# Kernel optimization log

Measured on AMD Instinct MI355X. Metric: run time of the kernel, lower is better.

Reference implementation:

```python
import jax, jax.numpy as jnp
import numpy as np

N_NODES, HIDDEN, LATENT, T_STEPS, BATCH, N_HEADS, N_LAYERS = 512, 64, 256, 10, 64, 4, 2
LN_EPS = 1e-5


def _layer_norm(x, g, b):
    mu = x.mean(-1, keepdims=True)
    var = ((x - mu) ** 2).mean(-1, keepdims=True)
    return (x - mu) * jax.lax.rsqrt(var + LN_EPS) * g + b


def _encoder_layer(x, in_w, in_b, out_w, out_b, l1_w, l1_b, l2_w, l2_b, g1, b1, g2, b2):
    # x: [S, B, D]; post-LN torch TransformerEncoderLayer, relu, no dropout (eval)
    S, B, D = x.shape
    hd = D // N_HEADS
    qkv = x @ in_w + in_b
    q, k, v = jnp.split(qkv, 3, axis=-1)
    q = q.reshape(S, B, N_HEADS, hd)
    k = k.reshape(S, B, N_HEADS, hd)
    v = v.reshape(S, B, N_HEADS, hd)
    att = jax.nn.softmax(jnp.einsum('sbhd,tbhd->bhst', q, k) / jnp.sqrt(jnp.float32(hd)), axis=-1)
    o = jnp.einsum('bhst,tbhd->sbhd', att, v).reshape(S, B, D) @ out_w + out_b
    x = _layer_norm(x + o, g1, b1)
    ff = jax.nn.relu(x @ l1_w + l1_b) @ l2_w + l2_b
    return _layer_norm(x + ff, g2, b2)


def _gru(x, w_ih, w_hh, b_ih, b_hh):
    # x: [B, T, I]; torch GRU gate order (r, z, n); returns all hidden states [B, T, H]
    Hh = w_hh.shape[0]
    gi = x @ w_ih + b_ih  # [B, T, 3H]

    def step(h, gi_t):
        gh = h @ w_hh + b_hh
        ir, iz, inn = jnp.split(gi_t, 3, -1)
        hr, hz, hn = jnp.split(gh, 3, -1)
        r = jax.nn.sigmoid(ir + hr)
        z = jax.nn.sigmoid(iz + hz)
        n = jnp.tanh(inn + r * hn)
        h_new = (1.0 - z) * n + z * h
        return h_new, h_new

    h0 = jnp.zeros((x.shape[0], Hh), x.dtype)
    _, out = jax.lax.scan(step, h0, jnp.swapaxes(gi, 0, 1))
    return jnp.swapaxes(out, 0, 1)


def _replace_zero(t):
    return jnp.where(t == 0.0, jnp.asarray(1e-8, t.dtype), t)


def _forward(X, Z, edge_score_now, edge_score_lag, prior_adj, wp1, bp1, enc_in_w, enc_in_b, enc_out_w, enc_out_b, enc_l1_w, enc_l1_b, enc_l2_w, enc_l2_b, enc_g1, enc_b1, enc_g2, enc_b2, wp2, bp2, fs_w, fs_b, ft_w, ft_b, gru_w_ih, gru_w_hh, gru_b_ih, gru_b_hh, tp_w, tp_b, ltn_w, ltn_b, gat_wl, gat_bl, gat_wr, gat_br, gat_att, gat_bias, gl_w, gl_b, time_context):
    # --- transformer encoder over time ---
    x = X @ wp1 + bp1                       # [B, T, H]
    x = jnp.transpose(x, (1, 0, 2))          # [T, B, H] (seq-first)
    for l in range(N_LAYERS):
        x = _encoder_layer(x, enc_in_w[l], enc_in_b[l], enc_out_w[l], enc_out_b[l], enc_l1_w[l], enc_l1_b[l], enc_l2_w[l], enc_l2_b[l], enc_g1[l], enc_b1[l], enc_g2[l], enc_b2[l])
    x = x @ wp2 + bp2                        # [T, B, N]
    x_inst = x[0]
    x_lag = x[1:].mean(0)
    # --- gumbel-softmax adjacency (tau=1, hard=False); fixed gumbel noise key ---
    k1, k2 = jax.random.split(jax.random.key(42))
    log_now = jnp.einsum('bk,bj->kj', x_inst, x_inst)
    log_lag = jax.nn.sigmoid(jnp.einsum('bk,bj->kj', x_lag, x_lag))
    a_now = jax.nn.softmax(log_now + jax.random.gumbel(k1, log_now.shape, log_now.dtype), -1)
    a_lag = jax.nn.softmax(log_lag + jax.random.gumbel(k2, log_lag.shape, log_lag.dtype), -1)
    adj_now = jnp.clip(jax.nn.sigmoid(edge_score_now + prior_adj + a_now), 0.0, 1.0)
    adj_lag = jnp.clip(jax.nn.sigmoid(edge_score_lag + prior_adj + a_lag), 0.0, 1.0)
    eye = jnp.eye(adj_now.shape[0], dtype=bool)
    adj_now = _replace_zero(jnp.where(eye, 0.0, adj_now))
    adj_lag = _replace_zero(jnp.where(eye, 0.0, adj_lag))
    # --- temporal RealNVP flow ---
    z1, z2 = jnp.split(Z, 2, axis=1)
    s = jax.nn.sigmoid(z1 @ fs_w + fs_b)
    z2 = s * z2 + (z1 @ ft_w + ft_b)
    freqs = jnp.exp(jnp.linspace(0.0, float(T_STEPS), LATENT // 2)).astype(Z.dtype)
    sin_in = time_context.astype(Z.dtype)[..., None] * freqs      # [N, T, L/2]
    temb = jnp.concatenate([jnp.sin(sin_in), jnp.cos(sin_in)], -1)  # [N, T, L]
    tout = _gru(temb, gru_w_ih, gru_w_hh, gru_b_ih, gru_b_hh)      # [N, T, L/2]
    z2 = z2 + jnp.einsum('btc,t->bc', tout, tp_w) + tp_b
    Zn = jnp.concatenate([z1, z2], 1) @ ltn_w + ltn_b              # [N, num_nodes]
    # --- GATv2 message passing; adj_now+adj_lag has no exact zeros (replace_zero),
    # so dense_to_sparse yields the fully connected edge set incl. self-loops ---
    Hh, C = gat_att.shape
    Nn = Zn.shape[0]
    xl = (Zn @ gat_wl + gat_bl).reshape(Nn, Hh, C)  # source features
    xr = (Zn @ gat_wr + gat_br).reshape(Nn, Hh, C)  # target features
    e = jnp.einsum('ijhc,hc->ijh', jax.nn.leaky_relu(xr[:, None] + xl[None, :], 0.2), gat_att)
    alpha = jax.nn.softmax(e, axis=1)                # softmax over source nodes j
    x_emb = jnp.einsum('ijh,jhc->ihc', alpha, xl).reshape(Nn, Hh * C) + gat_bias
    ml = x_emb @ gl_w + gl_b
    mean, log_var = jnp.split(ml, 2, -1)
    scale = jnp.exp(0.5 * jnp.clip(log_var, -5.0, 2.0))  # Laplace(mean, scale) params
    return adj_now, adj_lag, mean, scale


def setup_inputs() -> dict:
    key = jax.random.key(0)
    ks = iter(jax.random.split(key, 64))

    def rn(shape, scale=1.0):
        return jax.random.normal(next(ks), shape, jnp.float32) * scale

    N, Hd, L, T, B, nL = N_NODES, HIDDEN, LATENT, T_STEPS, BATCH, N_LAYERS
    d3 = 3 * Hd
    inp = dict(
        X=rn((B, T, N)),
        Z=rn((N, L)),
        edge_score_now=rn((N, N)),
        edge_score_lag=rn((N, N)),
        prior_adj=jnp.zeros((N, N), jnp.float32),
        wp1=rn((N, Hd), N ** -0.5), bp1=jnp.zeros((Hd,), jnp.float32),
        enc_in_w=rn((nL, Hd, d3), Hd ** -0.5), enc_in_b=jnp.zeros((nL, d3), jnp.float32),
        enc_out_w=rn((nL, Hd, Hd), Hd ** -0.5), enc_out_b=jnp.zeros((nL, Hd), jnp.float32),
        enc_l1_w=rn((nL, Hd, Hd), Hd ** -0.5), enc_l1_b=jnp.zeros((nL, Hd), jnp.float32),
        enc_l2_w=rn((nL, Hd, Hd), Hd ** -0.5), enc_l2_b=jnp.zeros((nL, Hd), jnp.float32),
        enc_g1=jnp.ones((nL, Hd), jnp.float32), enc_b1=jnp.zeros((nL, Hd), jnp.float32),
        enc_g2=jnp.ones((nL, Hd), jnp.float32), enc_b2=jnp.zeros((nL, Hd), jnp.float32),
        wp2=rn((Hd, N), Hd ** -0.5), bp2=jnp.zeros((N,), jnp.float32),
        fs_w=rn((L // 2, L // 2), (L // 2) ** -0.5), fs_b=jnp.zeros((L // 2,), jnp.float32),
        ft_w=rn((L // 2, L // 2), (L // 2) ** -0.5), ft_b=jnp.zeros((L // 2,), jnp.float32),
        gru_w_ih=rn((L, 3 * (L // 2)), L ** -0.5),
        gru_w_hh=rn((L // 2, 3 * (L // 2)), (L // 2) ** -0.5),
        gru_b_ih=jnp.zeros((3 * (L // 2),), jnp.float32),
        gru_b_hh=jnp.zeros((3 * (L // 2),), jnp.float32),
        tp_w=rn((T,), T ** -0.5), tp_b=jnp.zeros((1,), jnp.float32),
        ltn_w=rn((L, N), L ** -0.5), ltn_b=jnp.zeros((N,), jnp.float32),
        gat_wl=rn((N, 4 * Hd), N ** -0.5), gat_bl=jnp.zeros((4 * Hd,), jnp.float32),
        gat_wr=rn((N, 4 * Hd), N ** -0.5), gat_br=jnp.zeros((4 * Hd,), jnp.float32),
        gat_att=rn((4, Hd), Hd ** -0.5), gat_bias=jnp.zeros((4 * Hd,), jnp.float32),
        gl_w=rn((4 * Hd, 2 * N), (4 * Hd) ** -0.5), gl_b=jnp.zeros((2 * N,), jnp.float32),
        time_context=jax.random.randint(next(ks), (N, T), 0, 100, jnp.int32),
    )
    return inp


def reference(X, Z, edge_score_now, edge_score_lag, prior_adj, wp1, bp1, enc_in_w, enc_in_b, enc_out_w, enc_out_b, enc_l1_w, enc_l1_b, enc_l2_w, enc_l2_b, enc_g1, enc_b1, enc_g2, enc_b2, wp2, bp2, fs_w, fs_b, ft_w, ft_b, gru_w_ih, gru_w_hh, gru_b_ih, gru_b_hh, tp_w, tp_b, ltn_w, ltn_b, gat_wl, gat_bl, gat_wr, gat_br, gat_att, gat_bias, gl_w, gl_b, time_context):
    return _forward(X, Z, edge_score_now, edge_score_lag, prior_adj, wp1, bp1, enc_in_w, enc_in_b, enc_out_w, enc_out_b, enc_l1_w, enc_l1_b, enc_l2_w, enc_l2_b, enc_g1, enc_b1, enc_g2, enc_b2, wp2, bp2, fs_w, fs_b, ft_w, ft_b, gru_w_ih, gru_w_hh, gru_b_ih, gru_b_hh, tp_w, tp_b, ltn_w, ltn_b, gat_wl, gat_bl, gat_wr, gat_br, gat_att, gat_bias, gl_w, gl_b, time_context)
```

## Files before the change

### kernel.cpp

```cpp
#include <hip/hip_runtime.h>
#include <stdint.h>
#include <math.h>

#define NN 512
#define HID 64
#define LAT 256
#define TS 10
#define BAT 64

#define DEVFN static __device__ __forceinline__

DEVFN uint32_t rotl32(uint32_t v, int d) { return (v << d) | (v >> (32 - d)); }

DEVFN void threefry2x32(uint32_t k0, uint32_t k1, uint32_t x0, uint32_t x1,
                        uint32_t& o0, uint32_t& o1) {
  uint32_t ks0 = k0, ks1 = k1, ks2 = k0 ^ k1 ^ 0x1BD11BDAu;
  x0 += ks0; x1 += ks1;
  x0 += x1; x1 = rotl32(x1, 13); x1 ^= x0;
  x0 += x1; x1 = rotl32(x1, 15); x1 ^= x0;
  x0 += x1; x1 = rotl32(x1, 26); x1 ^= x0;
  x0 += x1; x1 = rotl32(x1, 6);  x1 ^= x0;
  x0 += ks1; x1 += ks2 + 1u;
  x0 += x1; x1 = rotl32(x1, 17); x1 ^= x0;
  x0 += x1; x1 = rotl32(x1, 29); x1 ^= x0;
  x0 += x1; x1 = rotl32(x1, 16); x1 ^= x0;
  x0 += x1; x1 = rotl32(x1, 24); x1 ^= x0;
  x0 += ks2; x1 += ks0 + 2u;
  x0 += x1; x1 = rotl32(x1, 13); x1 ^= x0;
  x0 += x1; x1 = rotl32(x1, 15); x1 ^= x0;
  x0 += x1; x1 = rotl32(x1, 26); x1 ^= x0;
  x0 += x1; x1 = rotl32(x1, 6);  x1 ^= x0;
  x0 += ks0; x1 += ks1 + 3u;
  x0 += x1; x1 = rotl32(x1, 17); x1 ^= x0;
  x0 += x1; x1 = rotl32(x1, 29); x1 ^= x0;
  x0 += x1; x1 = rotl32(x1, 16); x1 ^= x0;
  x0 += x1; x1 = rotl32(x1, 24); x1 ^= x0;
  x0 += ks1; x1 += ks2 + 4u;
  x0 += x1; x1 = rotl32(x1, 13); x1 ^= x0;
  x0 += x1; x1 = rotl32(x1, 15); x1 ^= x0;
  x0 += x1; x1 = rotl32(x1, 26); x1 ^= x0;
  x0 += x1; x1 = rotl32(x1, 6);  x1 ^= x0;
  x0 += ks2; x1 += ks0 + 5u;
  o0 = x0; o1 = x1;
}

DEVFN float sigmoidf_(float x) { return 1.0f / (1.0f + expf(-x)); }

DEVFN float gumbel_bits(uint32_t bits) {
  const float tiny = 1.17549435e-38f;
  float f = __uint_as_float((bits >> 9) | 0x3F800000u) - 1.0f;
  float u = f * (1.0f - tiny) + tiny;
  u = fmaxf(tiny, u);
  return -logf(-logf(u));
}

DEVFN float block_red256(float v, float* red, bool ismax) {
  #pragma unroll
  for (int o = 32; o > 0; o >>= 1) {
    float w = __shfl_down(v, o, 64);
    v = ismax ? fmaxf(v, w) : v + w;
  }
  if ((threadIdx.x & 63) == 0) red[threadIdx.x >> 6] = v;
  __syncthreads();
  float r = ismax ? fmaxf(fmaxf(red[0], red[1]), fmaxf(red[2], red[3]))
                  : ((red[0] + red[1]) + (red[2] + red[3]));
  __syncthreads();
  return r;
}

DEVFN float wave_red_sum64(float v) {
  #pragma unroll
  for (int o = 32; o > 0; o >>= 1) v += __shfl_xor(v, o, 64);
  return v;
}

#define ACC4(acc, x4, w4) { acc += (x4).x * (w4).x; acc += (x4).y * (w4).y; \
                            acc += (x4).z * (w4).z; acc += (x4).w * (w4).w; }

__global__ __launch_bounds__(384) void prep_kernel(
    const float* __restrict__ w_hh, float* __restrict__ w_hhT,
    const float* __restrict__ X, const float* __restrict__ wp1,
    const float* __restrict__ bp1, float* __restrict__ x0,
    const float* __restrict__ w_ih, const float* __restrict__ b_ih,
    float* __restrict__ gi_table,
    const float* __restrict__ Z, const float* __restrict__ fs_w,
    const float* __restrict__ fs_b, const float* __restrict__ ft_w,
    const float* __restrict__ ft_b, float* __restrict__ z2p) {
  const int tid = threadIdx.x;
  if (blockIdx.x < 128) {
    const int idx = blockIdx.x * 384 + tid;
    const int k4 = idx / 1536, rem = idx % 1536;
    const int t = rem >> 2, kl = rem & 3;
    w_hhT[idx] = w_hh[(k4 * 4 + kl) * 384 + t];
  } else if (blockIdx.x < 288) {
    const int r0 = (blockIdx.x - 128) * 4;
    const int g = tid >> 6, c = tid & 63;
    __shared__ float Xb[4][NN];
    __shared__ float Wb[128 * 64];
    for (int i = tid; i < 4 * NN; i += 384)
      Xb[i >> 9][i & 511] = X[r0 * NN + i];
    float acc = (tid < 256) ? bp1[c] : 0.0f;
    for (int ch = 0; ch < 4; ch++) {
      const int n0 = ch * 128;
      __syncthreads();
      for (int i = tid; i < 128 * 64; i += 384) {
        int k = i >> 6, cc = i & 63;
        Wb[((k >> 2) * 64 + cc) * 4 + (k & 3)] = wp1[(n0 + k) * 64 + cc];
      }
      __syncthreads();
      if (tid < 256) {
        #pragma unroll 8
        for (int n4 = 0; n4 < 32; n4++) {
          float4 w4 = *(const float4*)&Wb[(n4 * 64 + c) * 4];
          float4 x4 = *(const float4*)&Xb[g][n0 + n4 * 4];
          ACC4(acc, x4, w4);
        }
      }
    }
    if (tid < 256) x0[(r0 + g) * HID + c] = acc;
  } else if (blockIdx.x < 388) {
    const int v = blockIdx.x - 288;
    const int t = tid;
    __shared__ float temb[256];
    if (t < 256) {
      float fr = (float)exp((double)(t & 127) * (10.0 / 127.0));
      float arg = (float)v * fr;
      temb[t] = (t < 128) ? sinf(arg) : cosf(arg);
    }
    __syncthreads();
    float acc = b_ih[t];
    for (int k = 0; k < 256; k++) acc += temb[k] * w_ih[k * 384 + t];
    gi_table[v * 384 + t] = acc;
  } else {
    const int n = (blockIdx.x - 388) * 3 + (tid >> 7);
    const int c = tid & 127;
    __shared__ float z1s[3][128];
    if (n < NN) z1s[tid >> 7][c] = Z[n * LAT + c];
    __syncthreads();
    if (n < NN) {
      const float* z1 = z1s[tid >> 7];
      float a = fs_b[c], t = ft_b[c];
      for (int k = 0; k < 128; k++) {
        float zz = z1[k];
        a += zz * fs_w[k * 128 + c];
        t += zz * ft_w[k * 128 + c];
      }
      z2p[n * 128 + c] = sigmoidf_(a) * Z[n * LAT + 128 + c] + t;
    }
  }
}

__global__ __launch_bounds__(768) void encgru_kernel(
    const float* __restrict__ x0,
    const float* __restrict__ in_w, const float* __restrict__ in_b,
    const float* __restrict__ out_w, const float* __restrict__ out_b,
    const float* __restrict__ l1_w, const float* __restrict__ l1_b,
    const float* __restrict__ l2_w, const float* __restrict__ l2_b,
    const float* __restrict__ g1, const float* __restrict__ b1,
    const float* __restrict__ g2, const float* __restrict__ b2,
    float* __restrict__ x_enc,
    const int* __restrict__ tctx, const float* __restrict__ w_hhT4,
    const float* __restrict__ b_hh, const float* __restrict__ gi_table,
    const float* __restrict__ tp_w, const float* __restrict__ tp_b,
    const float* __restrict__ z2p, float* __restrict__ z2f) {
  __shared__ float smem[28176];
  const int tid = threadIdx.x;

  if (blockIdx.x < 64) {
    const int b = blockIdx.x;
    const int s = tid >> 6, c = tid & 63;
    float* WbA  = smem;
    float* WbB  = smem + 12288;
    float* xx   = smem + 24576;
    float* qkv  = smem + 25216;
    float* scb  = smem + 27136;
    float* tmpv = smem + 27536;

    if (tid < 640) xx[s * 64 + c] = x0[b * 640 + tid];

    for (int l = 0; l < 2; l++) {
      const float* inw = in_w + l * HID * 192; const float* inb = in_b + l * 192;
      const float* ow  = out_w + l * HID * HID; const float* ob = out_b + l * HID;
      const float* w1  = l1_w + l * HID * HID; const float* bb1 = l1_b + l * HID;
      const float* w2  = l2_w + l * HID * HID; const float* bb2 = l2_b + l * HID;
      const float* gg1 = g1 + l * HID; const float* be1 = b1 + l * HID;
      const float* gg2 = g2 + l * HID; const float* be2 = b2 + l * HID;

      __syncthreads();
      for (int i = tid; i < 12288; i += 768) {
        int k = i / 192, cc = i % 192;
        WbA[((k >> 2) * 192 + cc) * 4 + (k & 3)] = inw[i];
      }
      for (int i = tid; i < 12288; i += 768) {
        int m = i >> 12, rem = i & 4095, k = rem >> 6, cc = rem & 63;
        float v = (m == 0) ? ow[rem] : (m == 1) ? w1[rem] : w2[rem];
        WbB[m * 4096 + ((k >> 2) * 64 + cc) * 4 + (k & 3)] = v;
      }
      __syncthreads();

      if (tid < 640) {
        #pragma unroll
        for (int part = 0; part < 3; part++) {
          const int cc = part * 64 + c;
          float acc = inb[cc];
          #pragma unroll
          for (int k4 = 0; k4 < 16; k4++) {
            float4 w4 = *(const float4*)&WbA[(k4 * 192 + cc) * 4];
            float4 x4 = *(const float4*)&xx[s * 64 + k4 * 4];
            ACC4(acc, x4, w4);
          }
          qkv[s * 192 + cc] = acc;
        }
      }
      __syncthreads();

      if (tid < 40) {
        const int h = tid / 10, r = tid % 10;
        float e[10];
        for (int t = 0; t < 10; t++) {
          float acc = 0.0f;
          for (int d = 0; d < 16; d++)
            acc += qkv[r * 192 + h * 16 + d] * qkv[t * 192 + 64 + h * 16 + d];
          e[t] = acc * 0.25f;
        }
        float m = -1e30f;
        for (int t = 0; t < 10; t++) m = fmaxf(m, e[t]);
        float sum = 0.0f;
        for (int t = 0; t < 10; t++) { e[t] = expf(e[t] - m); sum += e[t]; }
        float inv = 1.0f / sum;
        for (int t = 0; t < 10; t++) scb[h * 100 + r * 10 + t] = e[t] * inv;
      }
      __syncthreads();

      float v1 = 0.0f;
      if (tid < 640) {
        const int h = c >> 4;
        float acc = 0.0f;
        for (int t = 0; t < 10; t++)
          acc += scb[h * 100 + s * 10 + t] * qkv[t * 192 + 128 + c];
        tmpv[s * 64 + c] = acc;
      }
      __threadfence_block();
      if (tid < 640) {
        float acc = ob[c] + xx[s * 64 + c];
        #pragma unroll
        for (int k4 = 0; k4 < 16; k4++) {
          float4 w4 = *(const float4*)&WbB[(k4 * 64 + c) * 4];
          float4 x4 = *(const float4*)&tmpv[s * 64 + k4 * 4];
          ACC4(acc, x4, w4);
        }
        float mu = wave_red_sum64(acc) * (1.0f / 64.0f);
        float d = acc - mu;
        float var = wave_red_sum64(d * d) * (1.0f / 64.0f);
        float rs = rsqrtf(var + 1e-5f);
        v1 = d * rs * gg1[c] + be1[c];
        xx[s * 64 + c] = v1;
      }
      __threadfence_block();
      if (tid < 640) {
        float acc = bb1[c];
        #pragma unroll
        for (int k4 = 0; k4 < 16; k4++) {
          float4 w4 = *(const float4*)&WbB[4096 + (k4 * 64 + c) * 4];
          float4 x4 = *(const float4*)&xx[s * 64 + k4 * 4];
          ACC4(acc, x4, w4);
        }
        tmpv[s * 64 + c] = fmaxf(acc, 0.0f);
      }
      __threadfence_block();
      if (tid < 640) {
        float acc = bb2[c] + v1;
        #pragma unroll
        for (int k4 = 0; k4 < 16; k4++) {
          float4 w4 = *(const float4*)&WbB[8192 + (k4 * 64 + c) * 4];
          float4 x4 = *(const float4*)&tmpv[s * 64 + k4 * 4];
          ACC4(acc, x4, w4);
        }
        float mu = wave_red_sum64(acc) * (1.0f / 64.0f);
        float d = acc - mu;
        float var = wave_red_sum64(d * d) * (1.0f / 64.0f);
        float rs = rsqrtf(var + 1e-5f);
        xx[s * 64 + c] = d * rs * gg2[c] + be2[c];
      }
      __threadfence_block();
    }
    if (tid < 640) x_enc[b * 640 + tid] = xx[s * 64 + c];
  } else {
    const int n0 = (blockIdx.x - 64) * 4;
    const int half = tid >= 384 ? 1 : 0;
    const int c = tid - half * 384;
    float* h      = smem;
    float* part   = smem + 512;
    float* gi_lds = smem + 3584;
    float* tpw    = smem + 18944;
    for (int i = tid; i < 4 * TS * 384; i += 768) {
      int g = i / 3840, rem = i % 3840, s = rem / 384, col = rem % 384;
      gi_lds[(g * TS + s) * 384 + col] = gi_table[tctx[(n0 + g) * 10 + s] * 384 + col];
    }
    if (tid < TS) tpw[tid] = tp_w[tid];
    const float4* wbase = (const float4*)w_hhT4 + (half * 16) * 384 + c;
    const float bhh = (half == 0) ? b_hh[c] : 0.0f;
    float acc_tp = 0.0f;
    if (tid < 512) h[tid] = 0.0f;
    __syncthreads();
    #pragma unroll
    for (int s = 0; s < 10; s++) {
      float accs[4];
      #pragma unroll
      for (int g = 0; g < 4; g++) accs[g] = bhh;
      #pragma unroll
      for (int k4 = 0; k4 < 16; k4++) {
        float4 w4 = wbase[k4 * 384];
        #pragma unroll
        for (int g = 0; g < 4; g++) {
          float4 hv = *(const float4*)&h[g * 128 + (half * 16 + k4) * 4];
          ACC4(accs[g], hv, w4);
        }
      }
      #pragma unroll
      for (int g = 0; g < 4; g++) part[(half * 4 + g) * 384 + c] = accs[g];
      __syncthreads();
      if (tid < 512) {
        const int g = tid >> 7, cc = tid & 127;
        const float* gi = gi_lds + (g * TS + s) * 384;
        float gh_r = part[g * 384 + cc]           + part[(4 + g) * 384 + cc];
        float gh_z = part[g * 384 + 128 + cc]     + part[(4 + g) * 384 + 128 + cc];
        float gh_n = part[g * 384 + 256 + cc]     + part[(4 + g) * 384 + 256 + cc];
        float r = sigmoidf_(gi[cc] + gh_r);
        float z = sigmoidf_(gi[128 + cc] + gh_z);
        float nn2 = tanhf(gi[256 + cc] + r * gh_n);
        float hn = (1.0f - z) * nn2 + z * h[g * 128 + cc];
        h[g * 128 + cc] = hn;
        acc_tp += hn * tpw[s];
      }
      __syncthreads();
    }
    if (tid < 512) {
      const int g = tid >> 7, cc = tid & 127;
      z2f[(n0 + g) * 128 + cc] = z2p[(n0 + g) * 128 + cc] + acc_tp + tp_b[0];
    }
  }
}

__global__ __launch_bounds__(256) void wp2zna_kernel(
    const float* __restrict__ x_enc, const float* __restrict__ wp2,
    const float* __restrict__ bp2,
    float* __restrict__ x_inst, float* __restrict__ x_lag,
    const float* __restrict__ Z, const float* __restrict__ z2f,
    const float* __restrict__ ltn_w, const float* __restrict__ ltn_b,
    float* __restrict__ zn_ws) {
  const int tid = threadIdx.x;
  if (blockIdx.x < 128) {
    const int b = blockIdx.x >> 1, half = blockIdx.x & 1;
    const int n = half * 256 + tid;
    __shared__ float xxl[640];
    __shared__ float Wb[32 * 256];
    for (int i = tid; i < 640; i += 256) xxl[i] = x_enc[b * 640 + i];
    float accs[10];
    #pragma unroll
    for (int si = 0; si < 10; si++) accs[si] = 0.0f;
    for (int ch = 0; ch < 2; ch++) {
      __syncthreads();
      for (int i = tid; i < 32 * 256; i += 256)
        Wb[i] = wp2[(ch * 32 + (i >> 8)) * NN + half * 256 + (i & 255)];
      __syncthreads();
      for (int k = 0; k < 32; k++) {
        float w = Wb[k * 256 + tid];
        #pragma unroll
        for (int si = 0; si < 10; si++) accs[si] += xxl[si * 64 + ch * 32 + k] * w;
      }
    }
    float bias = bp2[n];
    x_inst[b * NN + n] = accs[0] + bias;
    float lag = 0.0f;
    for (int si = 1; si < 10; si++) lag += accs[si];
    x_lag[b * NN + n] = lag * (1.0f / 9.0f) + bias;
  } else {
    const int bid = blockIdx.x - 128;
    const int nt = bid >> 2, cg = bid & 3;
    const int oo = tid & 127, gsel = tid >> 7;
    const int o = cg * 128 + oo;
    const int n0 = nt * 4;
    __shared__ float zcat[4][LAT];
    for (int i = tid; i < 4 * LAT; i += 256) {
      int g = i >> 8, k = i & 255;
      zcat[g][k] = (k < 128) ? Z[(n0 + g) * LAT + k] : z2f[(n0 + g) * 128 + (k - 128)];
    }
    __syncthreads();
    const float bias = ltn_b[o];
    float accA = bias, accB = bias;
    const int g0 = gsel, g1 = gsel + 2;
    for (int k = 0; k < LAT; k++) {
      float w = ltn_w[k * NN + o];
      accA += zcat[g0][k] * w;
      accB += zcat[g1][k] * w;
    }
    zn_ws[(n0 + g0) * NN + o] = accA;
    zn_ws[(n0 + g1) * NN + o] = accB;
  }
}

__global__ __launch_bounds__(256) void adjznb_kernel(
    const float* __restrict__ x_inst, const float* __restrict__ x_lag,
    const float* __restrict__ es_now, const float* __restrict__ es_lag,
    const float* __restrict__ prior, float* __restrict__ out,
    const float* __restrict__ zn_ws,
    const float* __restrict__ wl, const float* __restrict__ bl,
    const float* __restrict__ wr, const float* __restrict__ br,
    float* __restrict__ xl, float* __restrict__ xr) {
  const int tid = threadIdx.x;
  if (blockIdx.x < 1024) {
    const int k = blockIdx.x & 511;
    const int v = blockIdx.x >> 9;
    const float* xs = v ? x_lag : x_inst;
    const float* es = v ? es_lag : es_now;
    __shared__ float ck[BAT];
    __shared__ float red[4];
    if (tid < BAT) ck[tid] = xs[tid * NN + k];
    __syncthreads();
    uint32_t ka, kb, t0, t1;
    threefry2x32(0u, 42u, 0u, (uint32_t)v, ka, kb);
    float vals[2];
    #pragma unroll
    for (int jj = 0; jj < 2; jj++) {
      int j = tid + jj * 256;
      float acc = 0.0f;
      for (int bb = 0; bb < BAT; bb++) acc += ck[bb] * xs[bb * NN + j];
      if (v) acc = sigmoidf_(acc);
      threefry2x32(ka, kb, 0u, (uint32_t)(k * NN + j), t0, t1);
      vals[jj] = acc + gumbel_bits(t0 ^ t1);
    }
    float m = block_red256(fmaxf(vals[0], vals[1]), red, true);
    float e0 = expf(vals[0] - m), e1 = expf(vals[1] - m);
    float s = block_red256(e0 + e1, red, false);
    float inv = 1.0f / s;
    #pragma unroll
    for (int jj = 0; jj < 2; jj++) {
      int j = tid + jj * 256;
      float a = (jj ? e1 : e0) * inv;
      float t = es[k * NN + j] + prior[k * NN + j] + a;
      float sg = sigmoidf_(t);
      sg = fminf(fmaxf(sg, 0.0f), 1.0f);
      if (j == k) sg = 0.0f;
      if (sg == 0.0f) sg = 1e-8f;
      out[v * NN * NN + k * NN + j] = sg;
    }
  } else {
    const int bid = blockIdx.x - 1024;
    const int nt = bid >> 2, cg = bid & 3;
    const int o = cg * 64 + (tid & 63), g = tid >> 6;
    const int n = nt * 4 + g;
    __shared__ float znr[4][NN];
    for (int i = tid; i < 4 * NN; i += 256)
      znr[i >> 9][i & 511] = zn_ws[(nt * 4 + (i >> 9)) * NN + (i & 511)];
    __syncthreads();
    float accL = bl[o], accR = br[o];
    for (int k = 0; k < NN; k++) {
      float z = znr[g][k];
      accL += z * wl[k * 256 + o];
      accR += z * wr[k * 256 + o];
    }
    xl[n * 256 + o] = accL;
    xr[n * 256 + o] = accR;
  }
}

__global__ __launch_bounds__(256) void gatE4_kernel(
    const float* __restrict__ xl, const float* __restrict__ xr,
    const float* __restrict__ attw, float* __restrict__ e_ws) {
  const int b = blockIdx.x;
  const int jt = b & 7, h = (b >> 3) & 3, it = b >> 5;
  const int tid = threadIdx.x;
  const int i_l = tid >> 4, jq = tid & 15;
  __shared__ float xlt[64][68];
  __shared__ float xrt[16][68];
  __shared__ float awl[64];
  for (int idx = tid; idx < 1024; idx += 256) {
    int j = idx >> 4, c4 = idx & 15;
    float4 v = *(const float4*)&xl[(jt * 64 + j) * 256 + h * 64 + c4 * 4];
    xlt[c4 * 4 + 0][j] = v.x;
    xlt[c4 * 4 + 1][j] = v.y;
    xlt[c4 * 4 + 2][j] = v.z;
    xlt[c4 * 4 + 3][j] = v.w;
  }
  for (int idx = tid; idx < 1024; idx += 256) {
    int i = idx >> 6, cc = idx & 63;
    xrt[i][cc] = xr[(it * 16 + i) * 256 + h * 64 + cc];
  }
  if (tid < 64) awl[tid] = attw[h * 64 + tid];
  __syncthreads();
  float acc0 = 0.0f, acc1 = 0.0f, acc2 = 0.0f, acc3 = 0.0f;
  #pragma unroll
  for (int c4 = 0; c4 < 16; c4++) {
    float4 aw4 = *(const float4*)&awl[c4 * 4];
    float4 xr4 = *(const float4*)&xrt[i_l][c4 * 4];
    float4 xl0 = *(const float4*)&xlt[c4 * 4 + 0][jq * 4];
    float4 xl1 = *(const float4*)&xlt[c4 * 4 + 1][jq * 4];
    float4 xl2 = *(const float4*)&xlt[c4 * 4 + 2][jq * 4];
    float4 xl3 = *(const float4*)&xlt[c4 * 4 + 3][jq * 4];
    {
      float v0 = xr4.x + xl0.x; v0 = (v0 >= 0.0f) ? v0 : 0.2f * v0;
      float v1 = xr4.x + xl0.y; v1 = (v1 >= 0.0f) ? v1 : 0.2f * v1;
      float v2 = xr4.x + xl0.z; v2 = (v2 >= 0.0f) ? v2 : 0.2f * v2;
      float v3 = xr4.x + xl0.w; v3 = (v3 >= 0.0f) ? v3 : 0.2f * v3;
      acc0 += v0 * aw4.x; acc1 += v1 * aw4.x; acc2 += v2 * aw4.x; acc3 += v3 * aw4.x;
    }
    {
      float v0 = xr4.y + xl1.x; v0 = (v0 >= 0.0f) ? v0 : 0.2f * v0;
      float v1 = xr4.y + xl1.y; v1 = (v1 >= 0.0f) ? v1 : 0.2f * v1;
      float v2 = xr4.y + xl1.z; v2 = (v2 >= 0.0f) ? v2 : 0.2f * v2;
      float v3 = xr4.y + xl1.w; v3 = (v3 >= 0.0f) ? v3 : 0.2f * v3;
      acc0 += v0 * aw4.y; acc1 += v1 * aw4.y; acc2 += v2 * aw4.y; acc3 += v3 * aw4.y;
    }
    {
      float v0 = xr4.z + xl2.x; v0 = (v0 >= 0.0f) ? v0 : 0.2f * v0;
      float v1 = xr4.z + xl2.y; v1 = (v1 >= 0.0f) ? v1 : 0.2f * v1;
      float v2 = xr4.z + xl2.z; v2 = (v2 >= 0.0f) ? v2 : 0.2f * v2;
      float v3 = xr4.z + xl2.w; v3 = (v3 >= 0.0f) ? v3 : 0.2f * v3;
      acc0 += v0 * aw4.z; acc1 += v1 * aw4.z; acc2 += v2 * aw4.z; acc3 += v3 * aw4.z;
    }
    {
      float v0 = xr4.w + xl3.x; v0 = (v0 >= 0.0f) ? v0 : 0.2f * v0;
      float v1 = xr4.w + xl3.y; v1 = (v1 >= 0.0f) ? v1 : 0.2f * v1;
      float v2 = xr4.w + xl3.z; v2 = (v2 >= 0.0f) ? v2 : 0.2f * v2;
      float v3 = xr4.w + xl3.w; v3 = (v3 >= 0.0f) ? v3 : 0.2f * v3;
      acc0 += v0 * aw4.w; acc1 += v1 * aw4.w; acc2 += v2 * aw4.w; acc3 += v3 * aw4.w;
    }
  }
  const int i = it * 16 + i_l;
  float* dst = e_ws + i * 2048 + h * 512 + jt * 64 + jq * 4;
  dst[0] = acc0; dst[1] = acc1; dst[2] = acc2; dst[3] = acc3;
}

__global__ __launch_bounds__(256) void gatSX_kernel(
    const float* __restrict__ e_ws, const float* __restrict__ xl,
    const float* __restrict__ gbias, float* __restrict__ xemb) {
  const int it = blockIdx.x >> 2, h = blockIdx.x & 3;
  const int tid = threadIdx.x;
  const int cq = tid & 15, jp = (tid >> 4) & 3, ip = tid >> 6;
  __shared__ float al[4][512];
  __shared__ float red[4];
  for (int i = tid; i < 4 * 512; i += 256)
    al[i >> 9][i & 511] = e_ws[(it * 4 + (i >> 9)) * 2048 + h * 512 + (i & 511)];
  __syncthreads();
  #pragma unroll
  for (int ii = 0; ii < 4; ii++) {
    float v0 = al[ii][tid], v1 = al[ii][256 + tid];
    float m = block_red256(fmaxf(v0, v1), red, true);
    float e0 = expf(v0 - m), e1 = expf(v1 - m);
    float ssum = block_red256(e0 + e1, red, false);
    float inv = 1.0f / ssum;
    al[ii][tid] = e0 * inv;
    al[ii][256 + tid] = e1 * inv;
  }
  __syncthreads();
  float acc0 = 0.0f, acc1 = 0.0f, acc2 = 0.0f, acc3 = 0.0f;
  #pragma unroll 4
  for (int js = 0; js < 128; js++) {
    const int j = js * 4 + jp;
    float4 x4 = *(const float4*)&xl[j * 256 + h * 64 + cq * 4];
    float a = al[ip][j];
    acc0 += a * x4.x; acc1 += a * x4.y; acc2 += a * x4.z; acc3 += a * x4.w;
  }
  acc0 += __shfl_xor(acc0, 16, 64); acc0 += __shfl_xor(acc0, 32, 64);
  acc1 += __shfl_xor(acc1, 16, 64); acc1 += __shfl_xor(acc1, 32, 64);
  acc2 += __shfl_xor(acc2, 16, 64); acc2 += __shfl_xor(acc2, 32, 64);
  acc3 += __shfl_xor(acc3, 16, 64); acc3 += __shfl_xor(acc3, 32, 64);
  if (jp == 0) {
    const int i = it * 4 + ip;
    const int o = h * 64 + cq * 4;
    float4 v = make_float4(acc0 + gbias[o],     acc1 + gbias[o + 1],
                           acc2 + gbias[o + 2], acc3 + gbias[o + 3]);
    *(float4*)&xemb[i * 256 + o] = v;
  }
}

__global__ __launch_bounds__(256) void gat_fused_kernel(
    const float* __restrict__ xl, const float* __restrict__ xr,
    const float* __restrict__ attw, const float* __restrict__ gbias,
    float* __restrict__ xemb) {
  const int i0 = blockIdx.x * 2, tid = threadIdx.x;
  __shared__ float xri[2][256];
  __shared__ float aw[256];
  __shared__ float e[2][4][NN];
  __shared__ float part[4][2][256];
  __shared__ float red[4];
  xri[0][tid] = xr[i0 * 256 + tid];
  xri[1][tid] = xr[(i0 + 1) * 256 + tid];
  aw[tid] = attw[tid];
  __syncthreads();
  #pragma unroll
  for (int jj = 0; jj < 2; jj++) {
    const int j = tid + jj * 256;
    const float4* xl4 = (const float4*)(xl + j * 256);
    #pragma unroll
    for (int hh = 0; hh < 4; hh++) {
      float accA = 0.0f, accB = 0.0f;
      #pragma unroll 4
      for (int c4 = 0; c4 < 16; c4++) {
        float4 v = xl4[hh * 16 + c4];
        const int cb = hh * 64 + c4 * 4;
        float w0 = aw[cb + 0], w1 = aw[cb + 1], w2 = aw[cb + 2], w3 = aw[cb + 3];
        float a0 = xri[0][cb + 0] + v.x; a0 = (a0 >= 0.0f) ? a0 : 0.2f * a0;
        float a1 = xri[0][cb + 1] + v.y; a1 = (a1 >= 0.0f) ? a1 : 0.2f * a1;
        float a2 = xri[0][cb + 2] + v.z; a2 = (a2 >= 0.0f) ? a2 : 0.2f * a2;
        float a3 = xri[0][cb + 3] + v.w; a3 = (a3 >= 0.0f) ? a3 : 0.2f * a3;
        accA += a0 * w0; accA += a1 * w1; accA += a2 * w2; accA += a3 * w3;
        float b0 = xri[1][cb + 0] + v.x; b0 = (b0 >= 0.0f) ? b0 : 0.2f * b0;
        float b1 = xri[1][cb + 1] + v.y; b1 = (b1 >= 0.0f) ? b1 : 0.2f * b1;
        float b2 = xri[1][cb + 2] + v.z; b2 = (b2 >= 0.0f) ? b2 : 0.2f * b2;
        float b3 = xri[1][cb + 3] + v.w; b3 = (b3 >= 0.0f) ? b3 : 0.2f * b3;
        accB += b0 * w0; accB += b1 * w1; accB += b2 * w2; accB += b3 * w3;
      }
      e[0][hh][j] = accA;
      e[1][hh][j] = accB;
    }
  }
  __syncthreads();
  for (int ii = 0; ii < 2; ii++) {
    for (int hh = 0; hh < 4; hh++) {
      float v0 = e[ii][hh][tid], v1 = e[ii][hh][tid + 256];
      float m = block_red256(fmaxf(v0, v1), red, true);
      float e0 = expf(v0 - m), e1 = expf(v1 - m);
      float ssum = block_red256(e0 + e1, red, false);
      float inv = 1.0f / ssum;
      e[ii][hh][tid] = e0 * inv;
      e[ii][hh][tid + 256] = e1 * inv;
    }
  }
  __syncthreads();
  {
    const int w = tid >> 6, lane = tid & 63;
    float a0 = 0.0f, a1 = 0.0f, a2 = 0.0f, a3 = 0.0f;
    float b0 = 0.0f, b1 = 0.0f, b2 = 0.0f, b3 = 0.0f;
    const int j0 = w * 128;
    for (int j = j0; j < j0 + 128; j++) {
      const float* xlr = xl + j * 256 + lane;
      float x0 = xlr[0], x1 = xlr[64], x2 = xlr[128], x3 = xlr[192];
      a0 += e[0][0][j] * x0; a1 += e[0][1][j] * x1;
      a2 += e[0][2][j] * x2; a3 += e[0][3][j] * x3;
      b0 += e[1][0][j] * x0; b1 += e[1][1][j] * x1;
      b2 += e[1][2][j] * x2; b3 += e[1][3][j] * x3;
    }
    part[w][0][lane]       = a0;
    part[w][0][64 + lane]  = a1;
    part[w][0][128 + lane] = a2;
    part[w][0][192 + lane] = a3;
    part[w][1][lane]       = b0;
    part[w][1][64 + lane]  = b1;
    part[w][1][128 + lane] = b2;
    part[w][1][192 + lane] = b3;
  }
  __syncthreads();
  {
    float accA = ((part[0][0][tid] + part[1][0][tid]) + part[2][0][tid]) + part[3][0][tid];
    float accB = ((part[0][1][tid] + part[1][1][tid]) + part[2][1][tid]) + part[3][1][tid];
    float gb = gbias[tid];
    xemb[i0 * 256 + tid] = accA + gb;
    xemb[(i0 + 1) * 256 + tid] = accB + gb;
  }
}

__global__ __launch_bounds__(256) void glgemm_kernel(
    const float* __restrict__ xemb, const float* __restrict__ gl_w,
    const float* __restrict__ gl_b, float* __restrict__ out_mean,
    float* __restrict__ out_scale) {
  const int ct = blockIdx.x & 15, it = blockIdx.x >> 4;
  const int tid = threadIdx.x;
  const int i0 = it * 16, col = ct * 64 + (tid & 63), ti = tid >> 6;
  __shared__ float xe[16][LAT];
  for (int o = tid; o < 16 * LAT; o += 256) {
    xe[o >> 8][o & 255] = xemb[(i0 + (o >> 8)) * LAT + (o & 255)];
  }
  __syncthreads();
  const float bias = gl_b[col];
  float acc0 = bias, acc1 = bias, acc2 = bias, acc3 = bias;
  const int r0 = ti * 4;
  #pragma unroll 4
  for (int k = 0; k < LAT; k++) {
    float w = gl_w[k * 1024 + col];
    acc0 += xe[r0 + 0][k] * w;
    acc1 += xe[r0 + 1][k] * w;
    acc2 += xe[r0 + 2][k] * w;
    acc3 += xe[r0 + 3][k] * w;
  }
  float accs[4] = {acc0, acc1, acc2, acc3};
  if (col < 512) {
    #pragma unroll
    for (int q = 0; q < 4; q++) out_mean[(i0 + r0 + q) * NN + col] = accs[q];
  } else {
    #pragma unroll
    for (int q = 0; q < 4; q++) {
      float lv = fminf(fmaxf(accs[q], -5.0f), 2.0f);
      out_scale[(i0 + r0 + q) * NN + (col - 512)] = expf(0.5f * lv);
    }
  }
}

extern "C" void kernel_launch(void* const* d_in, const int* in_sizes, int n_in,
                              void* d_out, int out_size, void* d_ws, size_t ws_size,
                              hipStream_t stream) {
  (void)in_sizes; (void)n_in; (void)out_size;
  const float* X        = (const float*)d_in[0];
  const float* Z        = (const float*)d_in[1];
  const float* es_now   = (const float*)d_in[2];
  const float* es_lag   = (const float*)d_in[3];
  const float* prior    = (const float*)d_in[4];
  const float* wp1      = (const float*)d_in[5];
  const float* bp1      = (const float*)d_in[6];
  const float* enc_in_w = (const float*)d_in[7];
  const float* enc_in_b = (const float*)d_in[8];
  const float* enc_out_w= (const float*)d_in[9];
  const float* enc_out_b= (const float*)d_in[10];
  const float* enc_l1_w = (const float*)d_in[11];
  const float* enc_l1_b = (const float*)d_in[12];
  const float* enc_l2_w = (const float*)d_in[13];
  const float* enc_l2_b = (const float*)d_in[14];
  const float* enc_g1   = (const float*)d_in[15];
  const float* enc_b1   = (const float*)d_in[16];
  const float* enc_g2   = (const float*)d_in[17];
  const float* enc_b2   = (const float*)d_in[18];
  const float* wp2      = (const float*)d_in[19];
  const float* bp2      = (const float*)d_in[20];
  const float* fs_w     = (const float*)d_in[21];
  const float* fs_b     = (const float*)d_in[22];
  const float* ft_w     = (const float*)d_in[23];
  const float* ft_b     = (const float*)d_in[24];
  const float* gru_w_ih = (const float*)d_in[25];
  const float* gru_w_hh = (const float*)d_in[26];
  const float* gru_b_ih = (const float*)d_in[27];
  const float* gru_b_hh = (const float*)d_in[28];
  const float* tp_w     = (const float*)d_in[29];
  const float* tp_b     = (const float*)d_in[30];
  const float* ltn_w    = (const float*)d_in[31];
  const float* ltn_b    = (const float*)d_in[32];
  const float* gat_wl   = (const float*)d_in[33];
  const float* gat_bl   = (const float*)d_in[34];
  const float* gat_wr   = (const float*)d_in[35];
  const float* gat_br   = (const float*)d_in[36];
  const float* gat_att  = (const float*)d_in[37];
  const float* gat_bias = (const float*)d_in[38];
  const float* gl_w     = (const float*)d_in[39];
  const float* gl_b     = (const float*)d_in[40];
  const int*   tctx     = (const int*)d_in[41];

  float* out = (float*)d_out;
  float* ws  = (float*)d_ws;
  float* x_inst   = ws;
  float* x_lag    = ws + 32768;
  float* z2p      = ws + 65536;
  float* z2f      = ws + 131072;
  float* xl       = ws + 196608;
  float* xr       = ws + 327680;
  float* gi_table = ws + 458752;
  float* xemb     = ws + 497152;
  float* x0       = ws + 628224;
  float* x_enc    = ws + 669184;
  float* zn_ws    = ws + 710144;
  float* e_ws     = ws + 972288;
  float* w_hhT4   = zn_ws;

  const bool big_ws = ws_size >= (size_t)(972288 + 512 * 2048) * 4;

  prep_kernel<<<dim3(559), dim3(384), 0, stream>>>(
      gru_w_hh, w_hhT4, X, wp1, bp1, x0,
      gru_w_ih, gru_b_ih, gi_table,
      Z, fs_w, fs_b, ft_w, ft_b, z2p);
  encgru_kernel<<<dim3(192), dim3(768), 0, stream>>>(
      x0, enc_in_w, enc_in_b, enc_out_w, enc_out_b,
      enc_l1_w, enc_l1_b, enc_l2_w, enc_l2_b,
      enc_g1, enc_b1, enc_g2, enc_b2, x_enc,
      tctx, w_hhT4, gru_b_hh, gi_table, tp_w, tp_b, z2p, z2f);
  wp2zna_kernel<<<dim3(640), dim3(256), 0, stream>>>(
      x_enc, wp2, bp2, x_inst, x_lag, Z, z2f, ltn_w, ltn_b, zn_ws);
  adjznb_kernel<<<dim3(1536), dim3(256), 0, stream>>>(
      x_inst, x_lag, es_now, es_lag, prior, out,
      zn_ws, gat_wl, gat_bl, gat_wr, gat_br, xl, xr);
  if (big_ws) {
    gatE4_kernel<<<dim3(1024), dim3(256), 0, stream>>>(xl, xr, gat_att, e_ws);
    gatSX_kernel<<<dim3(512), dim3(256), 0, stream>>>(e_ws, xl, gat_bias, xemb);
  } else {
    gat_fused_kernel<<<dim3(NN / 2), dim3(256), 0, stream>>>(
        xl, xr, gat_att, gat_bias, xemb);
  }
  glgemm_kernel<<<dim3(512), dim3(256), 0, stream>>>(
      xemb, gl_w, gl_b, out + 2 * NN * NN, out + 3 * NN * NN);
}
```

Measured before the change: 165.7 us.

## Fuse GAT attention scores, softmax, aggregation and output GEMM into one kernel

Replaces the separate GAT score, softmax/aggregate and output-linear kernels with a single kernel. Each block owns four target nodes, tiles xl through shared memory to compute edge scores, applies the softmax, aggregates, and then runs the gl_w GEMM directly from shared memory. This removes two kernel launches and the global round trips for the score matrix and xemb. The cost is only 128 blocks for the whole GAT stage, a large shared-memory footprint (about 106 KB), and every block re-reading all of xl and gl_w, which may leave the GPU under-occupied.

Measured after the change: 252.7 us. 52.5% more time.

```diff
diff --git a/kernel.cpp b/kernel.cpp
--- a/kernel.cpp
+++ b/kernel.cpp
@@ -465,234 +465,102 @@
   }
 }
 
-__global__ __launch_bounds__(256) void gatE4_kernel(
-    const float* __restrict__ xl, const float* __restrict__ xr,
-    const float* __restrict__ attw, float* __restrict__ e_ws) {
-  const int b = blockIdx.x;
-  const int jt = b & 7, h = (b >> 3) & 3, it = b >> 5;
-  const int tid = threadIdx.x;
-  const int i_l = tid >> 4, jq = tid & 15;
-  __shared__ float xlt[64][68];
-  __shared__ float xrt[16][68];
-  __shared__ float awl[64];
-  for (int idx = tid; idx < 1024; idx += 256) {
-    int j = idx >> 4, c4 = idx & 15;
-    float4 v = *(const float4*)&xl[(jt * 64 + j) * 256 + h * 64 + c4 * 4];
-    xlt[c4 * 4 + 0][j] = v.x;
-    xlt[c4 * 4 + 1][j] = v.y;
-    xlt[c4 * 4 + 2][j] = v.z;
-    xlt[c4 * 4 + 3][j] = v.w;
-  }
-  for (int idx = tid; idx < 1024; idx += 256) {
-    int i = idx >> 6, cc = idx & 63;
-    xrt[i][cc] = xr[(it * 16 + i) * 256 + h * 64 + cc];
-  }
-  if (tid < 64) awl[tid] = attw[h * 64 + tid];
-  __syncthreads();
-  float acc0 = 0.0f, acc1 = 0.0f, acc2 = 0.0f, acc3 = 0.0f;
-  #pragma unroll
-  for (int c4 = 0; c4 < 16; c4++) {
-    float4 aw4 = *(const float4*)&awl[c4 * 4];
-    float4 xr4 = *(const float4*)&xrt[i_l][c4 * 4];
-    float4 xl0 = *(const float4*)&xlt[c4 * 4 + 0][jq * 4];
-    float4 xl1 = *(const float4*)&xlt[c4 * 4 + 1][jq * 4];
-    float4 xl2 = *(const float4*)&xlt[c4 * 4 + 2][jq * 4];
-    float4 xl3 = *(const float4*)&xlt[c4 * 4 + 3][jq * 4];
-    {
-      float v0 = xr4.x + xl0.x; v0 = (v0 >= 0.0f) ? v0 : 0.2f * v0;
-      float v1 = xr4.x + xl0.y; v1 = (v1 >= 0.0f) ? v1 : 0.2f * v1;
-      float v2 = xr4.x + xl0.z; v2 = (v2 >= 0.0f) ? v2 : 0.2f * v2;
-      float v3 = xr4.x + xl0.w; v3 = (v3 >= 0.0f) ? v3 : 0.2f * v3;
-      acc0 += v0 * aw4.x; acc1 += v1 * aw4.x; acc2 += v2 * aw4.x; acc3 += v3 * aw4.x;
-    }
-    {
-      float v0 = xr4.y + xl1.x; v0 = (v0 >= 0.0f) ? v0 : 0.2f * v0;
-      float v1 = xr4.y + xl1.y; v1 = (v1 >= 0.0f) ? v1 : 0.2f * v1;
-      float v2 = xr4.y + xl1.z; v2 = (v2 >= 0.0f) ? v2 : 0.2f * v2;
-      float v3 = xr4.y + xl1.w; v3 = (v3 >= 0.0f) ? v3 : 0.2f * v3;
-      acc0 += v0 * aw4.y; acc1 += v1 * aw4.y; acc2 += v2 * aw4.y; acc3 += v3 * aw4.y;
-    }
-    {
-      float v0 = xr4.z + xl2.x; v0 = (v0 >= 0.0f) ? v0 : 0.2f * v0;
-      float v1 = xr4.z + xl2.y; v1 = (v1 >= 0.0f) ? v1 : 0.2f * v1;
-      float v2 = xr4.z + xl2.z; v2 = (v2 >= 0.0f) ? v2 : 0.2f * v2;
-      float v3 = xr4.z + xl2.w; v3 = (v3 >= 0.0f) ? v3 : 0.2f * v3;
-      acc0 += v0 * aw4.z; acc1 += v1 * aw4.z; acc2 += v2 * aw4.z; acc3 += v3 * aw4.z;
-    }
-    {
-      float v0 = xr4.w + xl3.x; v0 = (v0 >= 0.0f) ? v0 : 0.2f * v0;
-      float v1 = xr4.w + xl3.y; v1 = (v1 >= 0.0f) ? v1 : 0.2f * v1;
-      float v2 = xr4.w + xl3.z; v2 = (v2 >= 0.0f) ? v2 : 0.2f * v2;
-      float v3 = xr4.w + xl3.w; v3 = (v3 >= 0.0f) ? v3 : 0.2f * v3;
-      acc0 += v0 * aw4.w; acc1 += v1 * aw4.w; acc2 += v2 * aw4.w; acc3 += v3 * aw4.w;
-    }
-  }
-  const int i = it * 16 + i_l;
-  float* dst = e_ws + i * 2048 + h * 512 + jt * 64 + jq * 4;
-  dst[0] = acc0; dst[1] = acc1; dst[2] = acc2; dst[3] = acc3;
-}
-
-__global__ __launch_bounds__(256) void gatSX_kernel(
-    const float* __restrict__ e_ws, const float* __restrict__ xl,
-    const float* __restrict__ gbias, float* __restrict__ xemb) {
-  const int it = blockIdx.x >> 2, h = blockIdx.x & 3;
-  const int tid = threadIdx.x;
-  const int cq = tid & 15, jp = (tid >> 4) & 3, ip = tid >> 6;
-  __shared__ float al[4][512];
-  __shared__ float red[4];
-  for (int i = tid; i < 4 * 512; i += 256)
-    al[i >> 9][i & 511] = e_ws[(it * 4 + (i >> 9)) * 2048 + h * 512 + (i & 511)];
-  __syncthreads();
-  #pragma unroll
-  for (int ii = 0; ii < 4; ii++) {
-    float v0 = al[ii][tid], v1 = al[ii][256 + tid];
-    float m = block_red256(fmaxf(v0, v1), red, true);
-    float e0 = expf(v0 - m), e1 = expf(v1 - m);
-    float ssum = block_red256(e0 + e1, red, false);
-    float inv = 1.0f / ssum;
-    al[ii][tid] = e0 * inv;
-    al[ii][256 + tid] = e1 * inv;
-  }
-  __syncthreads();
-  float acc0 = 0.0f, acc1 = 0.0f, acc2 = 0.0f, acc3 = 0.0f;
-  #pragma unroll 4
-  for (int js = 0; js < 128; js++) {
-    const int j = js * 4 + jp;
-    float4 x4 = *(const float4*)&xl[j * 256 + h * 64 + cq * 4];
-    float a = al[ip][j];
-    acc0 += a * x4.x; acc1 += a * x4.y; acc2 += a * x4.z; acc3 += a * x4.w;
-  }
-  acc0 += __shfl_xor(acc0, 16, 64); acc0 += __shfl_xor(acc0, 32, 64);
-  acc1 += __shfl_xor(acc1, 16, 64); acc1 += __shfl_xor(acc1, 32, 64);
-  acc2 += __shfl_xor(acc2, 16, 64); acc2 += __shfl_xor(acc2, 32, 64);
-  acc3 += __shfl_xor(acc3, 16, 64); acc3 += __shfl_xor(acc3, 32, 64);
-  if (jp == 0) {
-    const int i = it * 4 + ip;
-    const int o = h * 64 + cq * 4;
-    float4 v = make_float4(acc0 + gbias[o],     acc1 + gbias[o + 1],
-                           acc2 + gbias[o + 2], acc3 + gbias[o + 3]);
-    *(float4*)&xemb[i * 256 + o] = v;
-  }
-}
-
-__global__ __launch_bounds__(256) void gat_fused_kernel(
+__global__ __launch_bounds__(256) void gatmega_kernel(
     const float* __restrict__ xl, const float* __restrict__ xr,
     const float* __restrict__ attw, const float* __restrict__ gbias,
-    float* __restrict__ xemb) {
-  const int i0 = blockIdx.x * 2, tid = threadIdx.x;
-  __shared__ float xri[2][256];
+    const float* __restrict__ gl_w, const float* __restrict__ gl_b,
+    float* __restrict__ out_mean, float* __restrict__ out_scale) {
+  const int i0 = blockIdx.x * 4;
+  const int tid = threadIdx.x;
+  __shared__ float xls[64][257];
+  __shared__ float e[4][4][512];
+  __shared__ float xr4[4][256];
   __shared__ float aw[256];
-  __shared__ float e[2][4][NN];
-  __shared__ float part[4][2][256];
+  __shared__ float xemb_l[4][256];
   __shared__ float red[4];
-  xri[0][tid] = xr[i0 * 256 + tid];
-  xri[1][tid] = xr[(i0 + 1) * 256 + tid];
+  for (int i = tid; i < 1024; i += 256)
+    xr4[i >> 8][i & 255] = xr[(i0 + (i >> 8)) * 256 + (i & 255)];
   aw[tid] = attw[tid];
+  for (int t = 0; t < 8; t++) {
+    __syncthreads();
+    for (int idx = tid; idx < 64 * 64; idx += 256) {
+      int j = idx >> 6, c4 = idx & 63;
+      float4 v = *(const float4*)&xl[(t * 64 + j) * 256 + c4 * 4];
+      xls[j][c4 * 4 + 0] = v.x;
+      xls[j][c4 * 4 + 1] = v.y;
+      xls[j][c4 * 4 + 2] = v.z;
+      xls[j][c4 * 4 + 3] = v.w;
+    }
+    __syncthreads();
+    #pragma unroll
+    for (int q = 0; q < 4; q++) {
+      const int idx = tid + q * 256;
+      const int r = idx >> 8;
+      const int h = (idx >> 6) & 3;
+      const int j = idx & 63;
+      float acc = 0.0f;
+      const int cb = h * 64;
+      for (int c = 0; c < 64; c++) {
+        float v = xr4[r][cb + c] + xls[j][cb + c];
+        v = (v >= 0.0f) ? v : 0.2f * v;
+        acc += v * aw[cb + c];
+      }
+      e[r][h][t * 64 + j] = acc;
+    }
+  }
   __syncthreads();
-  #pragma unroll
-  for (int jj = 0; jj < 2; jj++) {
-    const int j = tid + jj * 256;
-    const float4* xl4 = (const float4*)(xl + j * 256);
-    #pragma unroll
-    for (int hh = 0; hh < 4; hh++) {
-      float accA = 0.0f, accB = 0.0f;
-      #pragma unroll 4
-      for (int c4 = 0; c4 < 16; c4++) {
-        float4 v = xl4[hh * 16 + c4];
-        const int cb = hh * 64 + c4 * 4;
-        float w0 = aw[cb + 0], w1 = aw[cb + 1], w2 = aw[cb + 2], w3 = aw[cb + 3];
-        float a0 = xri[0][cb + 0] + v.x; a0 = (a0 >= 0.0f) ? a0 : 0.2f * a0;
-        float a1 = xri[0][cb + 1] + v.y; a1 = (a1 >= 0.0f) ? a1 : 0.2f * a1;
-        float a2 = xri[0][cb + 2] + v.z; a2 = (a2 >= 0.0f) ? a2 : 0.2f * a2;
-        float a3 = xri[0][cb + 3] + v.w; a3 = (a3 >= 0.0f) ? a3 : 0.2f * a3;
-        accA += a0 * w0; accA += a1 * w1; accA += a2 * w2; accA += a3 * w3;
-        float b0 = xri[1][cb + 0] + v.x; b0 = (b0 >= 0.0f) ? b0 : 0.2f * b0;
-        float b1 = xri[1][cb + 1] + v.y; b1 = (b1 >= 0.0f) ? b1 : 0.2f * b1;
-        float b2 = xri[1][cb + 2] + v.z; b2 = (b2 >= 0.0f) ? b2 : 0.2f * b2;
-        float b3 = xri[1][cb + 3] + v.w; b3 = (b3 >= 0.0f) ? b3 : 0.2f * b3;
-        accB += b0 * w0; accB += b1 * w1; accB += b2 * w2; accB += b3 * w3;
-      }
-      e[0][hh][j] = accA;
-      e[1][hh][j] = accB;
-    }
-  }
-  __syncthreads();
-  for (int ii = 0; ii < 2; ii++) {
-    for (int hh = 0; hh < 4; hh++) {
-      float v0 = e[ii][hh][tid], v1 = e[ii][hh][tid + 256];
+  for (int r = 0; r < 4; r++) {
+    for (int h = 0; h < 4; h++) {
+      float v0 = e[r][h][tid], v1 = e[r][h][tid + 256];
       float m = block_red256(fmaxf(v0, v1), red, true);
       float e0 = expf(v0 - m), e1 = expf(v1 - m);
       float ssum = block_red256(e0 + e1, red, false);
       float inv = 1.0f / ssum;
-      e[ii][hh][tid] = e0 * inv;
-      e[ii][hh][tid + 256] = e1 * inv;
+      e[r][h][tid] = e0 * inv;
+      e[r][h][tid + 256] = e1 * inv;
     }
   }
   __syncthreads();
   {
-    const int w = tid >> 6, lane = tid & 63;
+    const int h = tid >> 6;
     float a0 = 0.0f, a1 = 0.0f, a2 = 0.0f, a3 = 0.0f;
-    float b0 = 0.0f, b1 = 0.0f, b2 = 0.0f, b3 = 0.0f;
-    const int j0 = w * 128;
-    for (int j = j0; j < j0 + 128; j++) {
-      const float* xlr = xl + j * 256 + lane;
-      float x0 = xlr[0], x1 = xlr[64], x2 = xlr[128], x3 = xlr[192];
-      a0 += e[0][0][j] * x0; a1 += e[0][1][j] * x1;
-      a2 += e[0][2][j] * x2; a3 += e[0][3][j] * x3;
-      b0 += e[1][0][j] * x0; b1 += e[1][1][j] * x1;
-      b2 += e[1][2][j] * x2; b3 += e[1][3][j] * x3;
-    }
-    part[w][0][lane]       = a0;
-    part[w][0][64 + lane]  = a1;
-    part[w][0][128 + lane] = a2;
-    part[w][0][192 + lane] = a3;
-    part[w][1][lane]       = b0;
-    part[w][1][64 + lane]  = b1;
-    part[w][1][128 + lane] = b2;
-    part[w][1][192 + lane] = b3;
+    #pragma unroll 4
+    for (int j = 0; j < 512; j++) {
+      float x = xl[j * 256 + tid];
+      a0 += e[0][h][j] * x;
+      a1 += e[1][h][j] * x;
+      a2 += e[2][h][j] * x;
+      a3 += e[3][h][j] * x;
+    }
+    float gb = gbias[tid];
+    xemb_l[0][tid] = a0 + gb;
+    xemb_l[1][tid] = a1 + gb;
+    xemb_l[2][tid] = a2 + gb;
+    xemb_l[3][tid] = a3 + gb;
   }
   __syncthreads();
-  {
-    float accA = ((part[0][0][tid] + part[1][0][tid]) + part[2][0][tid]) + part[3][0][tid];
-    float accB = ((part[0][1][tid] + part[1][1][tid]) + part[2][1][tid]) + part[3][1][tid];
-    float gb = gbias[tid];
-    xemb[i0 * 256 + tid] = accA + gb;
-    xemb[(i0 + 1) * 256 + tid] = accB + gb;
-  }
-}
-
-__global__ __launch_bounds__(256) void glgemm_kernel(
-    const float* __restrict__ xemb, const float* __restrict__ gl_w,
-    const float* __restrict__ gl_b, float* __restrict__ out_mean,
-    float* __restrict__ out_scale) {
-  const int ct = blockIdx.x & 15, it = blockIdx.x >> 4;
-  const int tid = threadIdx.x;
-  const int i0 = it * 16, col = ct * 64 + (tid & 63), ti = tid >> 6;
-  __shared__ float xe[16][LAT];
-  for (int o = tid; o < 16 * LAT; o += 256) {
-    xe[o >> 8][o & 255] = xemb[(i0 + (o >> 8)) * LAT + (o & 255)];
-  }
-  __syncthreads();
-  const float bias = gl_b[col];
-  float acc0 = bias, acc1 = bias, acc2 = bias, acc3 = bias;
-  const int r0 = ti * 4;
-  #pragma unroll 4
-  for (int k = 0; k < LAT; k++) {
-    float w = gl_w[k * 1024 + col];
-    acc0 += xe[r0 + 0][k] * w;
-    acc1 += xe[r0 + 1][k] * w;
-    acc2 += xe[r0 + 2][k] * w;
-    acc3 += xe[r0 + 3][k] * w;
-  }
-  float accs[4] = {acc0, acc1, acc2, acc3};
-  if (col < 512) {
-    #pragma unroll
-    for (int q = 0; q < 4; q++) out_mean[(i0 + r0 + q) * NN + col] = accs[q];
-  } else {
-    #pragma unroll
-    for (int q = 0; q < 4; q++) {
-      float lv = fminf(fmaxf(accs[q], -5.0f), 2.0f);
-      out_scale[(i0 + r0 + q) * NN + (col - 512)] = expf(0.5f * lv);
+  #pragma unroll
+  for (int q = 0; q < 4; q++) {
+    const int col = tid + q * 256;
+    const float bias = gl_b[col];
+    float a0 = bias, a1 = bias, a2 = bias, a3 = bias;
+    for (int k = 0; k < 256; k++) {
+      float w = gl_w[k * 1024 + col];
+      a0 += xemb_l[0][k] * w;
+      a1 += xemb_l[1][k] * w;
+      a2 += xemb_l[2][k] * w;
+      a3 += xemb_l[3][k] * w;
+    }
+    float accs[4] = {a0, a1, a2, a3};
+    if (col < 512) {
+      #pragma unroll
+      for (int r = 0; r < 4; r++) out_mean[(i0 + r) * NN + col] = accs[r];
+    } else {
+      #pragma unroll
+      for (int r = 0; r < 4; r++) {
+        float lv = fminf(fmaxf(accs[r], -5.0f), 2.0f);
+        out_scale[(i0 + r) * NN + (col - 512)] = expf(0.5f * lv);
+      }
     }
   }
 }
@@ -700,7 +568,7 @@
 extern "C" void kernel_launch(void* const* d_in, const int* in_sizes, int n_in,
                               void* d_out, int out_size, void* d_ws, size_t ws_size,
                               hipStream_t stream) {
-  (void)in_sizes; (void)n_in; (void)out_size;
+  (void)in_sizes; (void)n_in; (void)out_size; (void)ws_size;
   const float* X        = (const float*)d_in[0];
   const float* Z        = (const float*)d_in[1];
   const float* es_now   = (const float*)d_in[2];
@@ -753,14 +621,10 @@
   float* xl       = ws + 196608;
   float* xr       = ws + 327680;
   float* gi_table = ws + 458752;
-  float* xemb     = ws + 497152;
   float* x0       = ws + 628224;
   float* x_enc    = ws + 669184;
   float* zn_ws    = ws + 710144;
-  float* e_ws     = ws + 972288;
   float* w_hhT4   = zn_ws;
-
-  const bool big_ws = ws_size >= (size_t)(972288 + 512 * 2048) * 4;
 
   prep_kernel<<<dim3(559), dim3(384), 0, stream>>>(
       gru_w_hh, w_hhT4, X, wp1, bp1, x0,
@@ -776,13 +640,7 @@
   adjznb_kernel<<<dim3(1536), dim3(256), 0, stream>>>(
       x_inst, x_lag, es_now, es_lag, prior, out,
       zn_ws, gat_wl, gat_bl, gat_wr, gat_br, xl, xr);
-  if (big_ws) {
-    gatE4_kernel<<<dim3(1024), dim3(256), 0, stream>>>(xl, xr, gat_att, e_ws);
-    gatSX_kernel<<<dim3(512), dim3(256), 0, stream>>>(e_ws, xl, gat_bias, xemb);
-  } else {
-    gat_fused_kernel<<<dim3(NN / 2), dim3(256), 0, stream>>>(
-        xl, xr, gat_att, gat_bias, xemb);
-  }
-  glgemm_kernel<<<dim3(512), dim3(256), 0, stream>>>(
-      xemb, gl_w, gl_b, out + 2 * NN * NN, out + 3 * NN * NN);
-}
+  gatmega_kernel<<<dim3(128), dim3(256), 0, stream>>>(
+      xl, xr, gat_att, gat_bias, gl_w, gl_b,
+      out + 2 * NN * NN, out + 3 * NN * NN);
+}
```
